# Performance work log

Measured on AMD Instinct MI355X. Metric: run time of the kernel, lower is better.

Reference implementation:

```python
import jax, jax.numpy as jnp
import numpy as np

BN_EPS = 1e-5

def setup_inputs() -> dict:
    key = jax.random.key(0)
    ks = jax.random.split(key, 10)
    B, Cin, Cout, H, W = 4, 256, 128, 64, 64
    Cqk = Cout // 8  # 16
    return {
        "x": jax.random.normal(ks[0], (B, Cin, H, W), dtype=jnp.float32),
        "conv_w": jax.random.normal(ks[1], (Cout, Cin, 3, 3), dtype=jnp.float32) * 0.03,
        "bn_gamma": jnp.ones((Cout,), dtype=jnp.float32),
        "bn_beta": jnp.zeros((Cout,), dtype=jnp.float32),
        "q_w": jax.random.normal(ks[2], (Cqk, Cout), dtype=jnp.float32) * 0.05,
        "q_b": jnp.zeros((Cqk,), dtype=jnp.float32),
        "k_w": jax.random.normal(ks[3], (Cqk, Cout), dtype=jnp.float32) * 0.05,
        "k_b": jnp.zeros((Cqk,), dtype=jnp.float32),
        "v_w": jax.random.normal(ks[4], (Cout, Cout), dtype=jnp.float32) * 0.05,
        "v_b": jnp.zeros((Cout,), dtype=jnp.float32),
        # gamma params are zero-init in the original; use small nonzero values so the
        # attention branches actually contribute (better correctness signal).
        "gamma_ca": jax.random.normal(ks[5], (1,), dtype=jnp.float32) * 0.1,
        "gamma_pa": jax.random.normal(ks[6], (1,), dtype=jnp.float32) * 0.1,
    }

def _conv_bn_relu(x, conv_w, bn_gamma, bn_beta):
    # 3x3 conv, stride 1, pad 1, no bias (NCHW / OIHW)
    y = jax.lax.conv_general_dilated(
        x, conv_w, window_strides=(1, 1), padding=((1, 1), (1, 1)),
        dimension_numbers=("NCHW", "OIHW", "NCHW"))
    # BatchNorm2d in training mode: batch statistics over (N, H, W)
    mean = jnp.mean(y, axis=(0, 2, 3), keepdims=True)
    var = jnp.var(y, axis=(0, 2, 3), keepdims=True)
    y = (y - mean) * jax.lax.rsqrt(var + BN_EPS)
    y = y * bn_gamma[None, :, None, None] + bn_beta[None, :, None, None]
    return jax.nn.relu(y)

def _cam(feat, gamma):
    B, C, H, W = feat.shape
    f = feat.reshape(B, C, H * W)                       # (B, C, N)
    energy = jnp.einsum("bcn,bdn->bcd", f, f)           # (B, C, C)
    energy_new = jnp.max(energy, axis=-1, keepdims=True) - energy
    attn = jnp.tanh(energy_new)
    out = jnp.einsum("bcd,bdn->bcn", attn, f).reshape(B, C, H, W)
    return gamma * out + feat

def _pam(feat, q_w, q_b, k_w, k_b, v_w, v_b, gamma):
    B, C, H, W = feat.shape
    N = H * W
    f = feat.reshape(B, C, N)
    q = jnp.einsum("oc,bcn->bon", q_w, f) + q_b[None, :, None]   # (B, C//8, N)
    k = jnp.einsum("oc,bcn->bon", k_w, f) + k_b[None, :, None]
    v = jnp.einsum("oc,bcn->bon", v_w, f) + v_b[None, :, None]   # (B, C, N)
    energy = jnp.einsum("bqn,bqm->bnm", q, k)                    # (B, N, N)
    attn = jnp.tanh(energy)
    # torch: bmm(value, attention^T): out[b,c,m] = sum_n v[b,c,n] * attn[b,m,n]
    out = jnp.einsum("bcn,bmn->bcm", v, attn).reshape(B, C, H, W)
    return gamma * out + feat

def reference(x, conv_w, bn_gamma, bn_beta, q_w, q_b, k_w, k_b, v_w, v_b, gamma_ca, gamma_pa):
    feat = _conv_bn_relu(x, conv_w, bn_gamma, bn_beta)
    out_ca = _cam(feat, gamma_ca)
    out_sa = _pam(feat, q_w, q_b, k_w, k_b, v_w, v_b, gamma_pa)
    return out_ca + out_sa + feat
```

## Files before the change

kernel.cpp:

```cpp
#include <hip/hip_runtime.h>
#include <math.h>

#define BATCH 4
#define CIN   256
#define CCH   128
#define HW    4096
#define CQK   16

using short8   = __attribute__((ext_vector_type(8))) short;
using floatx4  = __attribute__((ext_vector_type(4))) float;
using floatx16 = __attribute__((ext_vector_type(16))) float;
using uint4v   = __attribute__((ext_vector_type(4))) unsigned int;

__device__ __forceinline__ float fast_tanh(float x) {
    float e = __builtin_amdgcn_exp2f(x * 2.8853900817779268f);
    float r = __builtin_amdgcn_rcpf(e + 1.0f);
    return __builtin_fmaf(-2.0f, r, 1.0f);
}

__device__ __forceinline__ unsigned short f2bf(float f) {
    unsigned u = __float_as_uint(f);
    u += 0x7fff + ((u >> 16) & 1);
    return (unsigned short)(u >> 16);
}

__device__ __forceinline__ float bf2f(unsigned short u) {
    return __uint_as_float(((unsigned)u) << 16);
}

#define ROWMAP(r, hi) (((r) & 3) + (((r) >> 2) << 3) + ((hi) << 2))

#define XTP_ROW   (66 * 256)
#define XTP_BATCH (66 * 66 * 256)

__global__ __launch_bounds__(256) void prep_all_kernel(
        const float* __restrict__ x, const float* __restrict__ w,
        const float* __restrict__ qw, const float* __restrict__ qb,
        const float* __restrict__ kw, const float* __restrict__ kb,
        const float* __restrict__ vw, const float* __restrict__ vb,
        unsigned short* __restrict__ xTp, unsigned short* __restrict__ Wb2,
        unsigned short* __restrict__ Wqkv, float* __restrict__ biasAll,
        float* __restrict__ statsS, float* __restrict__ statsQ) {
    const int bx = blockIdx.x, tid = threadIdx.x;
    if (bx < 1024) {
        __shared__ unsigned short lds[64][72];
        const int ci0 = (bx & 3) << 6, yr = (bx >> 2) & 63, b = bx >> 8;
        const int cir = tid >> 2, xc = tid & 3;
        const float* xp = x + (((b << 8) + ci0 + cir) << 12) + (yr << 6) + xc * 16;
#pragma unroll
        for (int j = 0; j < 4; ++j) {
            float4 v = *(const float4*)(xp + j * 4);
            int xi = xc * 16 + j * 4;
            lds[xi + 0][cir] = f2bf(v.x);
            lds[xi + 1][cir] = f2bf(v.y);
            lds[xi + 2][cir] = f2bf(v.z);
            lds[xi + 3][cir] = f2bf(v.w);
        }
        const short8 z8 = (short8){0,0,0,0,0,0,0,0};
        if (tid < 16) {
            int col = (tid >> 3) ? 65 : 0;
            int part = tid & 7;
            *(short8*)(xTp + b * XTP_BATCH + (yr + 1) * XTP_ROW + col * 256 +
                       ci0 + part * 8) = z8;
        }
        if (yr == 0 || yr == 63) {
            int row = (yr == 0) ? 0 : 65;
            for (int e = tid; e < 528; e += 256) {
                int xi = e >> 3, part = e & 7;
                *(short8*)(xTp + b * XTP_BATCH + row * XTP_ROW + xi * 256 +
                           ci0 + part * 8) = z8;
            }
        }
        __syncthreads();
        const int xr = tid >> 2, part = tid & 3;
        unsigned short* dst = xTp + b * XTP_BATCH + (yr + 1) * XTP_ROW +
                              (xr + 1) * 256 + ci0 + part * 16;
        *(short8*)(dst + 0) = *(const short8*)&lds[xr][part * 16 + 0];
        *(short8*)(dst + 8) = *(const short8*)&lds[xr][part * 16 + 8];
    } else if (bx < 2176) {
        int o = (bx - 1024) * 256 + tid;
        int s   = o & 31;
        int co  = (o >> 5) & 127;
        int cc  = (o >> 12) & 7;
        int tap = o >> 15;
        int ci  = (cc << 5) + s;
        Wb2[o] = f2bf(w[co * 2304 + ci * 9 + tap]);
    } else if (bx < 2256) {
        int idx = (bx - 2176) * 256 + tid;
        int o = idx >> 7, c = idx & 127;
        float wv = (o < 16) ? qw[(o << 7) + c]
                 : (o < 32) ? kw[((o - 16) << 7) + c]
                            : vw[((o - 32) << 7) + c];
        Wqkv[idx] = f2bf(wv);
        if (idx < 160)
            biasAll[idx] = (idx < 16) ? qb[idx] : (idx < 32) ? kb[idx - 16] : vb[idx - 32];
    } else {
        if (tid < 128) { statsS[tid] = 0.f; statsQ[tid] = 0.f; }
    }
}

#define LOADBAND(R, KY)                                                        \
    {                                                                          \
        const unsigned short* g_ = bandbase + (KY) * XTP_ROW;                  \
        _Pragma("unroll")                                                      \
        for (int j = 0; j < 4; ++j)                                            \
            R[j] = *(const short8*)(g_ + ((tid + j * 256) << 3));              \
        if (tid < 64) R[4] = *(const short8*)(g_ + ((1024 + tid) << 3));       \
    }

#define WRITEBAND(R, BUF)                                                      \
    {                                                                          \
        char* p_ = (char*)&Bl[BUF][0];                                         \
        _Pragma("unroll")                                                      \
        for (int j = 0; j < 4; ++j) {                                          \
            int bb_ = (tid + j * 256) << 4;                                    \
            *(short8*)(p_ + (bb_ ^ (((bb_ >> 9) & 7) << 4))) = R[j];           \
        }                                                                      \
        if (tid < 64) {                                                        \
            int bb_ = (1024 + tid) << 4;                                       \
            *(short8*)(p_ + (bb_ ^ (((bb_ >> 9) & 7) << 4))) = R[4];           \
        }                                                                      \
    }

#define LOADA(P, TAP)                                                          \
    {                                                                          \
        const unsigned short* ar_ = Wb2 + ((TAP) << 15) + (aco0 << 5) + (quad << 3); \
        _Pragma("unroll")                                                      \
        for (int cc = 0; cc < 8; ++cc) {                                       \
            P[2 * cc]     = *(const short8*)(ar_ + (cc << 12));                \
            P[2 * cc + 1] = *(const short8*)(ar_ + (cc << 12) + 512);          \
        }                                                                      \
    }

#define CONVSTEP(BUF, KX, PC, PN, TAPN, PREF)                                  \
    {                                                                          \
        const char* bp_ = (const char*)&Bl[BUF][0];                            \
        const int pl0_ = l15 + (KX);                                           \
        const int sw_ = (pl0_ & 7) << 4;                                       \
        const int b0_ = (pl0_ << 9) + (quad << 4);                             \
        const int b1_ = b0_ + (16 << 9);                                       \
        const unsigned short* arn_ = Wb2 + ((TAPN) << 15) + (aco0 << 5) + (quad << 3); \
        _Pragma("unroll")                                                      \
        for (int cc = 0; cc < 8; ++cc) {                                       \
            if (PREF) {                                                        \
                PN[2 * cc]     = *(const short8*)(arn_ + (cc << 12));          \
                PN[2 * cc + 1] = *(const short8*)(arn_ + (cc << 12) + 512);    \
            }                                                                  \
            short8 bf0 = *(const short8*)(bp_ + ((b0_ + (cc << 6)) ^ sw_));    \
            short8 bf1 = *(const short8*)(bp_ + ((b1_ + (cc << 6)) ^ sw_));    \
            acc00 = __builtin_amdgcn_mfma_f32_16x16x32_bf16(PC[2 * cc], bf0, acc00, 0, 0, 0); \
            acc01 = __builtin_amdgcn_mfma_f32_16x16x32_bf16(PC[2 * cc], bf1, acc01, 0, 0, 0); \
            acc10 = __builtin_amdgcn_mfma_f32_16x16x32_bf16(PC[2 * cc + 1], bf0, acc10, 0, 0, 0); \
            acc11 = __builtin_amdgcn_mfma_f32_16x16x32_bf16(PC[2 * cc + 1], bf1, acc11, 0, 0, 0); \
        }                                                                      \
    }

__global__ __launch_bounds__(256, 2) void conv_mfma_kernel(
        const unsigned short* __restrict__ xTp, const unsigned short* __restrict__ Wb2,
        float* __restrict__ y, float* __restrict__ convP) {
    const int tid = threadIdx.x;
    const int w = tid >> 6, lane = tid & 63, l15 = lane & 15, quad = lane >> 4;
    const int idx = blockIdx.x;
    const int xcd = idx & 7, rr = idx >> 3;
    const int yl = rr & 7, ph = (rr >> 3) & 1, b = rr >> 4;
    const int yr = (xcd << 3) + yl;
    const int cobase = w << 5;
    const int px0 = ph << 5;
    const int aco0 = cobase + l15;

    __shared__ __align__(16) unsigned short Bl[2][8704];

    const unsigned short* bandbase = xTp + b * XTP_BATCH + yr * XTP_ROW + (px0 << 8);

    floatx4 acc00 = (floatx4){0.f, 0.f, 0.f, 0.f};
    floatx4 acc01 = (floatx4){0.f, 0.f, 0.f, 0.f};
    floatx4 acc10 = (floatx4){0.f, 0.f, 0.f, 0.f};
    floatx4 acc11 = (floatx4){0.f, 0.f, 0.f, 0.f};

    short8 r0[5], r1[5], r2[5];
    short8 AbA[16], AbB[16];

    LOADBAND(r0, 0);
    WRITEBAND(r0, 0);
    LOADBAND(r1, 1);
    LOADA(AbA, 0);
    __syncthreads();

    WRITEBAND(r1, 1);
    LOADBAND(r2, 2);
    CONVSTEP(0, 0, AbA, AbB, 1, 1)
    CONVSTEP(0, 1, AbB, AbA, 2, 1)
    CONVSTEP(0, 2, AbA, AbB, 3, 1)
    __syncthreads();

    WRITEBAND(r2, 0);
    CONVSTEP(1, 0, AbB, AbA, 4, 1)
    CONVSTEP(1, 1, AbA, AbB, 5, 1)
    CONVSTEP(1, 2, AbB, AbA, 6, 1)
    __syncthreads();

    CONVSTEP(0, 0, AbA, AbB, 7, 1)
    CONVSTEP(0, 1, AbB, AbA, 8, 1)
    CONVSTEP(0, 2, AbA, AbB, 0, 0)

#pragma unroll
    for (int ns = 0; ns < 2; ++ns) {
        int px = px0 + (ns << 4) + l15;
        floatx4 a0 = ns ? acc01 : acc00;
        floatx4 a1 = ns ? acc11 : acc10;
#pragma unroll
        for (int r = 0; r < 4; ++r) {
            int co0 = cobase + (quad << 2) + r;
            y[(((b << 7) + co0) << 12) + (yr << 6) + px] = a0[r];
            y[(((b << 7) + co0 + 16) << 12) + (yr << 6) + px] = a1[r];
        }
    }

#pragma unroll
    for (int ms = 0; ms < 2; ++ms) {
        floatx4 aa = ms ? acc10 : acc00;
        floatx4 ab = ms ? acc11 : acc01;
#pragma unroll
        for (int r = 0; r < 4; ++r) {
            float s = aa[r] + ab[r];
            float q = aa[r] * aa[r] + ab[r] * ab[r];
#pragma unroll
            for (int off = 1; off < 16; off <<= 1) {
                s += __shfl_xor(s, off);
                q += __shfl_xor(q, off);
            }
            if (l15 == 0) {
                int co = cobase + ms * 16 + (quad << 2) + r;
                convP[(co << 9) + idx] = s;
                convP[((128 + co) << 9) + idx] = q;
            }
        }
    }
}

__global__ __launch_bounds__(64) void stats_reduce_kernel(
        const float* __restrict__ convP, float* __restrict__ statsS,
        float* __restrict__ statsQ) {
    const int s = blockIdx.x, t = threadIdx.x;
    const float* p = convP + (s << 9);
    float v = 0.f;
#pragma unroll
    for (int j = 0; j < 8; ++j) v += p[t + (j << 6)];
#pragma unroll
    for (int off = 32; off; off >>= 1) v += __shfl_xor(v, off);
    if (t == 0) {
        if (s < 128) statsS[s] = v;
        else         statsQ[s - 128] = v;
    }
}

__global__ __launch_bounds__(256) void bn_apply_kernel(
        const float* __restrict__ y, const float* __restrict__ statsS,
        const float* __restrict__ statsQ, const float* __restrict__ gamma,
        const float* __restrict__ beta, unsigned short* __restrict__ featB,
        unsigned short* __restrict__ fT) {
    __shared__ unsigned short lds[64][72];
    const int tid = threadIdx.x;
    const int c0 = blockIdx.x * 64, n0 = blockIdx.y * 64, b = blockIdx.z;
    const int cir = tid >> 2, xc = tid & 3;
    const int c = c0 + cir;
    const float S = statsS[c], Q = statsQ[c];
    const float mean = S * (1.f / 16384.f);
    const float var  = Q * (1.f / 16384.f) - mean * mean;
    const float rstd = rsqrtf(var + 1e-5f);
    const float sc = gamma[c] * rstd;
    const float sh = beta[c] - mean * sc;
    const float* yp = y + (((b << 7) + c) << 12) + n0 + xc * 16;
    unsigned short* fp = featB + (((b << 7) + c) << 12) + n0 + xc * 16;
#pragma unroll
    for (int j = 0; j < 4; ++j) {
        float4 v = *(const float4*)(yp + j * 4);
        ushort4 o;
        o.x = f2bf(fmaxf(fmaf(v.x, sc, sh), 0.f));
        o.y = f2bf(fmaxf(fmaf(v.y, sc, sh), 0.f));
        o.z = f2bf(fmaxf(fmaf(v.z, sc, sh), 0.f));
        o.w = f2bf(fmaxf(fmaf(v.w, sc, sh), 0.f));
        *(ushort4*)(fp + j * 4) = o;
        int ni = xc * 16 + j * 4;
        lds[ni + 0][cir] = o.x;
        lds[ni + 1][cir] = o.y;
        lds[ni + 2][cir] = o.z;
        lds[ni + 3][cir] = o.w;
    }
    __syncthreads();
    const int nr = tid >> 2, part = tid & 3;
    unsigned short* dst = fT + (((b << 12) + n0 + nr) << 7) + c0 + part * 16;
    *(short8*)(dst + 0) = *(const short8*)&lds[nr][part * 16 + 0];
    *(short8*)(dst + 8) = *(const short8*)&lds[nr][part * 16 + 8];
}

__global__ __launch_bounds__(256) void camqkv_kernel(
        const unsigned short* __restrict__ featB, float* __restrict__ ep,
        const unsigned short* __restrict__ Wqkv, const float* __restrict__ biasAll,
        const unsigned short* __restrict__ fT,
        unsigned short* __restrict__ qT, unsigned short* __restrict__ kT,
        unsigned short* __restrict__ vB) {
    const int bx = blockIdx.x, tid = threadIdx.x;
    const int l31 = tid & 31, hi = (tid >> 5) & 1;
    if (bx < 256) {
        const int kc = bx & 63, b = bx >> 6, wv = tid >> 6;
        floatx16 acc[4];
#pragma unroll
        for (int t = 0; t < 4; ++t)
#pragma unroll
            for (int r = 0; r < 16; ++r) acc[t][r] = 0.f;
        for (int s = 0; s < 4; ++s) {
            const int k0 = (kc << 6) + (s << 4) + (hi << 3);
            short8 fr = *(const short8*)&featB[(((b << 7) + (wv << 5) + l31) << 12) + k0];
            short8 fc0 = *(const short8*)&featB[(((b << 7) +  0 + l31) << 12) + k0];
            short8 fc1 = *(const short8*)&featB[(((b << 7) + 32 + l31) << 12) + k0];
            short8 fc2 = *(const short8*)&featB[(((b << 7) + 64 + l31) << 12) + k0];
            short8 fc3 = *(const short8*)&featB[(((b << 7) + 96 + l31) << 12) + k0];
            acc[0] = __builtin_amdgcn_mfma_f32_32x32x16_bf16(fr, fc0, acc[0], 0, 0, 0);
            acc[1] = __builtin_amdgcn_mfma_f32_32x32x16_bf16(fr, fc1, acc[1], 0, 0, 0);
            acc[2] = __builtin_amdgcn_mfma_f32_32x32x16_bf16(fr, fc2, acc[2], 0, 0, 0);
            acc[3] = __builtin_amdgcn_mfma_f32_32x32x16_bf16(fr, fc3, acc[3], 0, 0, 0);
        }
#pragma unroll
        for (int t = 0; t < 4; ++t)
#pragma unroll
            for (int r = 0; r < 16; ++r) {
                int c = ((tid >> 6) << 5) + ROWMAP(r, hi);
                int d = (t << 5) + l31;
                ep[(((kc << 2) + b) << 14) + (c << 7) + d] = acc[t][r];
            }
    } else {
        const int bi = bx - 256, b = bi >> 6, w = tid >> 6;
        const int n0 = ((bi & 63) << 6) + ((w >> 1) << 5);
        const int tstart = (w & 1) ? 3 : 0;
        const int tcnt   = (w & 1) ? 2 : 3;
        floatx16 acc[3];
#pragma unroll
        for (int t = 0; t < 3; ++t)
#pragma unroll
            for (int r = 0; r < 16; ++r) acc[t][r] = 0.f;
        for (int s = 0; s < 8; ++s) {
            const int k0 = (s << 4) + (hi << 3);
            short8 bf = *(const short8*)&fT[(((b << 12) + n0 + l31) << 7) + k0];
#pragma unroll
            for (int ti = 0; ti < 3; ++ti) {
                if (ti < tcnt) {
                    short8 aw = *(const short8*)&Wqkv[((((tstart + ti) << 5) + l31) << 7) + k0];
                    acc[ti] = __builtin_amdgcn_mfma_f32_32x32x16_bf16(aw, bf, acc[ti], 0, 0, 0);
                }
            }
        }
        const int n = n0 + l31;
#pragma unroll
        for (int ti = 0; ti < 3; ++ti) {
            if (ti >= tcnt) continue;
            const int t = tstart + ti;
#pragma unroll
            for (int r = 0; r < 16; ++r) {
                int o = (t << 5) + ROWMAP(r, hi);
                float val = acc[ti][r] + biasAll[o];
                if (t == 0) {
                    if (o < 16) qT[(((b << 12) + n) << 4) + o] = f2bf(val);
                    else        kT[(((b << 12) + n) << 4) + o - 16] = f2bf(val);
                } else if (o >= 32) {
                    vB[(((b << 7) + o - 32) << 12) + n] = f2bf(val);
                }
            }
        }
    }
}

#define PAM_STEP(LB, NC)                                                          \
    {                                                                             \
        const unsigned short* lb_ = (LB);                                         \
        const int na_ = nbase + ((NC) << 5);                                      \
        short8 avl0 = *(const short8*)(lb_ + ( l31       * 40) + hi * 8);         \
        short8 avh0 = *(const short8*)(lb_ + ( l31       * 40) + 16 + hi * 8);    \
        short8 avl1 = *(const short8*)(lb_ + ((32 + l31) * 40) + hi * 8);         \
        short8 avh1 = *(const short8*)(lb_ + ((32 + l31) * 40) + 16 + hi * 8);    \
        short8 avl2 = *(const short8*)(lb_ + ((64 + l31) * 40) + hi * 8);         \
        short8 avh2 = *(const short8*)(lb_ + ((64 + l31) * 40) + 16 + hi * 8);    \
        short8 avl3 = *(const short8*)(lb_ + ((96 + l31) * 40) + hi * 8);         \
        short8 avh3 = *(const short8*)(lb_ + ((96 + l31) * 40) + 16 + hi * 8);    \
        floatx16 s_ = __builtin_amdgcn_mfma_f32_32x32x16_bf16(ak, bq, zero16, 0, 0, 0); \
        if ((NC) < 31)                                                            \
            ak = *(const short8*)&kT[(((b << 12) + na_ + 32 + l31) << 4) + hi * 8]; \
        unsigned p_[8];                                                           \
        _Pragma("unroll")                                                         \
        for (int i = 0; i < 8; ++i) {                                             \
            float t0 = fast_tanh(s_[2 * i]);                                      \
            float t1 = fast_tanh(s_[2 * i + 1]);                                  \
            p_[i] = (__float_as_uint(t1) & 0xFFFF0000u) | (__float_as_uint(t0) >> 16); \
        }                                                                         \
        unsigned q0 = p_[0], q1 = p_[1], q2 = p_[2], q3 = p_[3];                  \
        unsigned q4 = p_[4], q5 = p_[5], q6 = p_[6], q7 = p_[7];                  \
        asm("v_permlane32_swap_b32 %0, %1" : "+v"(q0), "+v"(q2));                 \
        asm("v_permlane32_swap_b32 %0, %1" : "+v"(q1), "+v"(q3));                 \
        asm("v_permlane32_swap_b32 %0, %1" : "+v"(q4), "+v"(q6));                 \
        asm("v_permlane32_swap_b32 %0, %1" : "+v"(q5), "+v"(q7));                 \
        uint4v b1u, b2u;                                                          \
        b1u[0] = q0; b1u[1] = q1; b1u[2] = q2; b1u[3] = q3;                       \
        b2u[0] = q4; b2u[1] = q5; b2u[2] = q6; b2u[3] = q7;                       \
        short8 B1 = __builtin_bit_cast(short8, b1u);                              \
        short8 B2 = __builtin_bit_cast(short8, b2u);                              \
        __builtin_amdgcn_s_setprio(1);                                            \
        acc[0] = __builtin_amdgcn_mfma_f32_32x32x16_bf16(avl0, B1, acc[0], 0, 0, 0); \
        acc[0] = __builtin_amdgcn_mfma_f32_32x32x16_bf16(avh0, B2, acc[0], 0, 0, 0); \
        acc[1] = __builtin_amdgcn_mfma_f32_32x32x16_bf16(avl1, B1, acc[1], 0, 0, 0); \
        acc[1] = __builtin_amdgcn_mfma_f32_32x32x16_bf16(avh1, B2, acc[1], 0, 0, 0); \
        acc[2] = __builtin_amdgcn_mfma_f32_32x32x16_bf16(avl2, B1, acc[2], 0, 0, 0); \
        acc[2] = __builtin_amdgcn_mfma_f32_32x32x16_bf16(avh2, B2, acc[2], 0, 0, 0); \
        acc[3] = __builtin_amdgcn_mfma_f32_32x32x16_bf16(avl3, B1, acc[3], 0, 0, 0); \
        acc[3] = __builtin_amdgcn_mfma_f32_32x32x16_bf16(avh3, B2, acc[3], 0, 0, 0); \
        __builtin_amdgcn_s_setprio(0);                                            \
    }

__global__ __launch_bounds__(256) void pam_attn_kernel(
        const unsigned short* __restrict__ qT, const unsigned short* __restrict__ kT,
        const unsigned short* __restrict__ vB, unsigned short* __restrict__ pamP,
        const float* __restrict__ ep, unsigned short* __restrict__ attnB) {
    const int bx = blockIdx.x, tid = threadIdx.x;
    if (bx < 512) {
        const int nh = bx & 3, b = bx >> 7;
        const int w = tid >> 6, lane = tid & 63, l31 = lane & 31, hi = lane >> 5;
        const int m0 = (((bx >> 2) & 31) << 7) + (w << 5);

        __shared__ __align__(16) unsigned short vtile[2][5120];

        short8 bq = *(const short8*)&qT[(((b << 12) + m0 + l31) << 4) + hi * 8];

        floatx16 acc[4], zero16;
#pragma unroll
        for (int r = 0; r < 16; ++r) {
            acc[0][r] = 0.f; acc[1][r] = 0.f; acc[2][r] = 0.f; acc[3][r] = 0.f;
            zero16[r] = 0.f;
        }

        const int nbase = nh << 10;

        const int srow = tid >> 1, shalf = tid & 1;
        const unsigned short* vg = vB + (((b << 7) + srow) << 12) + nbase + shalf * 16;
        unsigned short* sw0 = &vtile[0][srow * 40 + shalf * 16];
        unsigned short* sw1 = &vtile[1][srow * 40 + shalf * 16];

        short8 ak = *(const short8*)&kT[(((b << 12) + nbase + l31) << 4) + hi * 8];

        short8 gA0 = *(const short8*)(vg + 0);
        short8 gA1 = *(const short8*)(vg + 8);
        short8 gB0 = *(const short8*)(vg + 32);
        short8 gB1 = *(const short8*)(vg + 40);
        *(short8*)(sw0 + 0) = gA0;
        *(short8*)(sw0 + 8) = gA1;

        for (int t = 0; t < 16; ++t) {
            const int e = t << 1;
            __syncthreads();
            *(short8*)(sw1 + 0) = gB0;
            *(short8*)(sw1 + 8) = gB1;
            if (t < 15) {
                gA0 = *(const short8*)(vg + (e + 2) * 32);
                gA1 = *(const short8*)(vg + (e + 2) * 32 + 8);
            }
            PAM_STEP(&vtile[0][0], e);
            __syncthreads();
            if (t < 15) {
                *(short8*)(sw0 + 0) = gA0;
                *(short8*)(sw0 + 8) = gA1;
                gB0 = *(const short8*)(vg + (e + 3) * 32);
                gB1 = *(const short8*)(vg + (e + 3) * 32 + 8);
            }
            PAM_STEP(&vtile[1][0], e + 1);
        }

        const int pbase = (((nh << 2) + b) << 19) + m0 + l31;
#pragma unroll
        for (int ct = 0; ct < 4; ++ct)
#pragma unroll
            for (int r = 0; r < 16; ++r) {
                int c = (ct << 5) + ROWMAP(r, hi);
                pamP[pbase + (c << 12)] = f2bf(acc[ct][r]);
            }
    } else {
        const int bi = bx - 512, b = bi >> 6;
        const int half = tid >> 7, t = tid & 127;
        const int c = ((bi & 63) << 1) + half;
        float v = 0.f;
#pragma unroll 8
        for (int s = 0; s < 64; ++s)
            v += ep[(((s << 2) + b) << 14) + (c << 7) + t];
        float m = v;
        for (int off = 32; off; off >>= 1) m = fmaxf(m, __shfl_down(m, off));
        __shared__ float mx[4];
        if ((tid & 63) == 0) mx[tid >> 6] = m;
        __syncthreads();
        float M = fmaxf(mx[half << 1], mx[(half << 1) + 1]);
        attnB[(b << 14) + (c << 7) + t] = f2bf(fast_tanh(M - v));
    }
}

__global__ __launch_bounds__(256) void combine_kernel(
        const unsigned short* __restrict__ attnB, const unsigned short* __restrict__ fT,
        const unsigned short* __restrict__ featB, const unsigned short* __restrict__ pamP,
        const float* __restrict__ gca, const float* __restrict__ gpa,
        float* __restrict__ out) {
    const int b = blockIdx.y, tid = threadIdx.x;
    const int w = tid >> 6, l31 = tid & 31, hi = (tid >> 5) & 1;
    const int m0 = (blockIdx.x << 6) + ((w >> 1) << 5);
    const int ct0 = (w & 1) << 1;
    floatx16 acc[2];
#pragma unroll
    for (int t = 0; t < 2; ++t)
#pragma unroll
        for (int r = 0; r < 16; ++r) acc[t][r] = 0.f;

    for (int s = 0; s < 8; ++s) {
        const int k0 = (s << 4) + (hi << 3);
        short8 bf = *(const short8*)&fT[(((b << 12) + m0 + l31) << 7) + k0];
        short8 a0 = *(const short8*)&attnB[(b << 14) + ((((ct0 + 0) << 5) + l31) << 7) + k0];
        short8 a1 = *(const short8*)&attnB[(b << 14) + ((((ct0 + 1) << 5) + l31) << 7) + k0];
        acc[0] = __builtin_amdgcn_mfma_f32_32x32x16_bf16(a0, bf, acc[0], 0, 0, 0);
        acc[1] = __builtin_amdgcn_mfma_f32_32x32x16_bf16(a1, bf, acc[1], 0, 0, 0);
    }
    const float gc = gca[0], gp = gpa[0];
    const int m = m0 + l31;
#pragma unroll
    for (int t = 0; t < 2; ++t)
#pragma unroll
        for (int r = 0; r < 16; ++r) {
            int c = ((ct0 + t) << 5) + ROWMAP(r, hi);
            int ci = (c << 12) + m;
            float p = bf2f(pamP[((0 * 4 + b) << 19) + ci]) +
                      bf2f(pamP[((1 * 4 + b) << 19) + ci]) +
                      bf2f(pamP[((2 * 4 + b) << 19) + ci]) +
                      bf2f(pamP[((3 * 4 + b) << 19) + ci]);
            float fb = bf2f(featB[(((b << 7) + c) << 12) + m]);
            out[(((b << 7) + c) << 12) + m] = 3.f * fb + gc * acc[t][r] + gp * p;
        }
}

extern "C" void kernel_launch(void* const* d_in, const int* in_sizes, int n_in,
                              void* d_out, int out_size, void* d_ws, size_t ws_size,
                              hipStream_t stream) {
    const float* x      = (const float*)d_in[0];
    const float* conv_w = (const float*)d_in[1];
    const float* bn_g   = (const float*)d_in[2];
    const float* bn_b   = (const float*)d_in[3];
    const float* q_w    = (const float*)d_in[4];
    const float* q_b    = (const float*)d_in[5];
    const float* k_w    = (const float*)d_in[6];
    const float* k_b    = (const float*)d_in[7];
    const float* v_w    = (const float*)d_in[8];
    const float* v_b    = (const float*)d_in[9];
    const float* gca    = (const float*)d_in[10];
    const float* gpa    = (const float*)d_in[11];
    float* out = (float*)d_out;

    float* ws = (float*)d_ws;
    float* convY  = ws;
    unsigned short* xTp = (unsigned short*)(ws + 2097152);
    float* ep     = ws + 4327424;
    unsigned short* Wb2  = (unsigned short*)(ws + 8521728);
    unsigned short* Wqkv = (unsigned short*)(ws + 8669184);
    float* statsS  = ws + 8679424;
    float* statsQ  = ws + 8679552;
    float* biasAll = ws + 8679680;
    unsigned short* attnB = (unsigned short*)(ws + 8679872);
    unsigned short* qT    = (unsigned short*)(ws + 8712640);
    unsigned short* kT    = (unsigned short*)(ws + 8843712);
    unsigned short* vB    = (unsigned short*)(ws + 8974784);
    unsigned short* featB = (unsigned short*)(ws + 10023360);
    unsigned short* fT    = (unsigned short*)(ws + 11071936);
    float* convP = ws + 4327424;
    unsigned short* pamP  = (unsigned short*)ws;

    prep_all_kernel<<<2257, 256, 0, stream>>>(x, conv_w, q_w, q_b, k_w, k_b,
                                              v_w, v_b, xTp, Wb2, Wqkv, biasAll,
                                              statsS, statsQ);
    conv_mfma_kernel<<<512, 256, 0, stream>>>(xTp, Wb2, convY, convP);
    stats_reduce_kernel<<<256, 64, 0, stream>>>(convP, statsS, statsQ);
    bn_apply_kernel<<<dim3(2, 64, 4), 256, 0, stream>>>(convY, statsS, statsQ,
                                                        bn_g, bn_b, featB, fT);
    camqkv_kernel<<<512, 256, 0, stream>>>(featB, ep, Wqkv, biasAll, fT, qT, kT, vB);
    pam_attn_kernel<<<768, 256, 0, stream>>>(qT, kT, vB, pamP, ep, attnB);
    combine_kernel<<<dim3(64, 4), 256, 0, stream>>>(attnB, fT, featB, pamP, gca, gpa, out);
}
```

Before: 171.8 us.

## Process two key chunks per pipeline stage to halve barriers and overlap tanh with MFMA

The PAM attention loop now stages two 32-column V chunks per shared-memory buffer and processes them in one step, halving the number of __syncthreads barriers. Inside a step, the second QK MFMA is issued before the first chunk's PV MFMAs, and its tanh runs afterwards, so VALU tanh work can overlap with matrix-core work. Shared memory per block doubles and register pressure rises from holding two sets of V fragments and scores, which may reduce occupancy.

```diff
diff --git a/kernel.cpp b/kernel.cpp
--- a/kernel.cpp
+++ b/kernel.cpp
@@ -370,48 +370,86 @@
     }
 }
 
-#define PAM_STEP(LB, NC)                                                          \
+#define PAM_STEP2(LB, NC0)                                                        \
     {                                                                             \
-        const unsigned short* lb_ = (LB);                                         \
-        const int na_ = nbase + ((NC) << 5);                                      \
-        short8 avl0 = *(const short8*)(lb_ + ( l31       * 40) + hi * 8);         \
-        short8 avh0 = *(const short8*)(lb_ + ( l31       * 40) + 16 + hi * 8);    \
-        short8 avl1 = *(const short8*)(lb_ + ((32 + l31) * 40) + hi * 8);         \
-        short8 avh1 = *(const short8*)(lb_ + ((32 + l31) * 40) + 16 + hi * 8);    \
-        short8 avl2 = *(const short8*)(lb_ + ((64 + l31) * 40) + hi * 8);         \
-        short8 avh2 = *(const short8*)(lb_ + ((64 + l31) * 40) + 16 + hi * 8);    \
-        short8 avl3 = *(const short8*)(lb_ + ((96 + l31) * 40) + hi * 8);         \
-        short8 avh3 = *(const short8*)(lb_ + ((96 + l31) * 40) + 16 + hi * 8);    \
-        floatx16 s_ = __builtin_amdgcn_mfma_f32_32x32x16_bf16(ak, bq, zero16, 0, 0, 0); \
-        if ((NC) < 31)                                                            \
-            ak = *(const short8*)&kT[(((b << 12) + na_ + 32 + l31) << 4) + hi * 8]; \
-        unsigned p_[8];                                                           \
+        const unsigned short* lbA_ = (LB);                                        \
+        const unsigned short* lbB_ = (LB) + 5120;                                 \
+        short8 aAl0 = *(const short8*)(lbA_ + ( l31       * 40) + hi * 8);        \
+        short8 aAh0 = *(const short8*)(lbA_ + ( l31       * 40) + 16 + hi * 8);   \
+        short8 aAl1 = *(const short8*)(lbA_ + ((32 + l31) * 40) + hi * 8);        \
+        short8 aAh1 = *(const short8*)(lbA_ + ((32 + l31) * 40) + 16 + hi * 8);   \
+        short8 aAl2 = *(const short8*)(lbA_ + ((64 + l31) * 40) + hi * 8);        \
+        short8 aAh2 = *(const short8*)(lbA_ + ((64 + l31) * 40) + 16 + hi * 8);   \
+        short8 aAl3 = *(const short8*)(lbA_ + ((96 + l31) * 40) + hi * 8);        \
+        short8 aAh3 = *(const short8*)(lbA_ + ((96 + l31) * 40) + 16 + hi * 8);   \
+        floatx16 sA_ = __builtin_amdgcn_mfma_f32_32x32x16_bf16(ak, bq, zero16, 0, 0, 0); \
+        ak = *(const short8*)&kT[(((b << 12) + nbase + (((NC0) + 1) << 5) + l31) << 4) + hi * 8]; \
+        short8 aBl0 = *(const short8*)(lbB_ + ( l31       * 40) + hi * 8);        \
+        short8 aBh0 = *(const short8*)(lbB_ + ( l31       * 40) + 16 + hi * 8);   \
+        short8 aBl1 = *(const short8*)(lbB_ + ((32 + l31) * 40) + hi * 8);        \
+        short8 aBh1 = *(const short8*)(lbB_ + ((32 + l31) * 40) + 16 + hi * 8);   \
+        short8 aBl2 = *(const short8*)(lbB_ + ((64 + l31) * 40) + hi * 8);        \
+        short8 aBh2 = *(const short8*)(lbB_ + ((64 + l31) * 40) + 16 + hi * 8);   \
+        short8 aBl3 = *(const short8*)(lbB_ + ((96 + l31) * 40) + hi * 8);        \
+        short8 aBh3 = *(const short8*)(lbB_ + ((96 + l31) * 40) + 16 + hi * 8);   \
+        unsigned pA_[8];                                                          \
         _Pragma("unroll")                                                         \
         for (int i = 0; i < 8; ++i) {                                             \
-            float t0 = fast_tanh(s_[2 * i]);                                      \
-            float t1 = fast_tanh(s_[2 * i + 1]);                                  \
-            p_[i] = (__float_as_uint(t1) & 0xFFFF0000u) | (__float_as_uint(t0) >> 16); \
+            float t0 = fast_tanh(sA_[2 * i]);                                     \
+            float t1 = fast_tanh(sA_[2 * i + 1]);                                 \
+            pA_[i] = (__float_as_uint(t1) & 0xFFFF0000u) | (__float_as_uint(t0) >> 16); \
         }                                                                         \
-        unsigned q0 = p_[0], q1 = p_[1], q2 = p_[2], q3 = p_[3];                  \
-        unsigned q4 = p_[4], q5 = p_[5], q6 = p_[6], q7 = p_[7];                  \
-        asm("v_permlane32_swap_b32 %0, %1" : "+v"(q0), "+v"(q2));                 \
-        asm("v_permlane32_swap_b32 %0, %1" : "+v"(q1), "+v"(q3));                 \
-        asm("v_permlane32_swap_b32 %0, %1" : "+v"(q4), "+v"(q6));                 \
-        asm("v_permlane32_swap_b32 %0, %1" : "+v"(q5), "+v"(q7));                 \
-        uint4v b1u, b2u;                                                          \
-        b1u[0] = q0; b1u[1] = q1; b1u[2] = q2; b1u[3] = q3;                       \
-        b2u[0] = q4; b2u[1] = q5; b2u[2] = q6; b2u[3] = q7;                       \
-        short8 B1 = __builtin_bit_cast(short8, b1u);                              \
-        short8 B2 = __builtin_bit_cast(short8, b2u);                              \
+        unsigned a0 = pA_[0], a1 = pA_[1], a2 = pA_[2], a3 = pA_[3];              \
+        unsigned a4 = pA_[4], a5 = pA_[5], a6 = pA_[6], a7 = pA_[7];              \
+        asm("v_permlane32_swap_b32 %0, %1" : "+v"(a0), "+v"(a2));                 \
+        asm("v_permlane32_swap_b32 %0, %1" : "+v"(a1), "+v"(a3));                 \
+        asm("v_permlane32_swap_b32 %0, %1" : "+v"(a4), "+v"(a6));                 \
+        asm("v_permlane32_swap_b32 %0, %1" : "+v"(a5), "+v"(a7));                 \
+        uint4v b1uA, b2uA;                                                        \
+        b1uA[0] = a0; b1uA[1] = a1; b1uA[2] = a2; b1uA[3] = a3;                   \
+        b2uA[0] = a4; b2uA[1] = a5; b2uA[2] = a6; b2uA[3] = a7;                   \
+        short8 B1A = __builtin_bit_cast(short8, b1uA);                            \
+        short8 B2A = __builtin_bit_cast(short8, b2uA);                            \
+        floatx16 sB_ = __builtin_amdgcn_mfma_f32_32x32x16_bf16(ak, bq, zero16, 0, 0, 0); \
+        if ((NC0) + 2 < 32)                                                       \
+            ak = *(const short8*)&kT[(((b << 12) + nbase + (((NC0) + 2) << 5) + l31) << 4) + hi * 8]; \
         __builtin_amdgcn_s_setprio(1);                                            \
-        acc[0] = __builtin_amdgcn_mfma_f32_32x32x16_bf16(avl0, B1, acc[0], 0, 0, 0); \
-        acc[0] = __builtin_amdgcn_mfma_f32_32x32x16_bf16(avh0, B2, acc[0], 0, 0, 0); \
-        acc[1] = __builtin_amdgcn_mfma_f32_32x32x16_bf16(avl1, B1, acc[1], 0, 0, 0); \
-        acc[1] = __builtin_amdgcn_mfma_f32_32x32x16_bf16(avh1, B2, acc[1], 0, 0, 0); \
-        acc[2] = __builtin_amdgcn_mfma_f32_32x32x16_bf16(avl2, B1, acc[2], 0, 0, 0); \
-        acc[2] = __builtin_amdgcn_mfma_f32_32x32x16_bf16(avh2, B2, acc[2], 0, 0, 0); \
-        acc[3] = __builtin_amdgcn_mfma_f32_32x32x16_bf16(avl3, B1, acc[3], 0, 0, 0); \
-        acc[3] = __builtin_amdgcn_mfma_f32_32x32x16_bf16(avh3, B2, acc[3], 0, 0, 0); \
+        acc[0] = __builtin_amdgcn_mfma_f32_32x32x16_bf16(aAl0, B1A, acc[0], 0, 0, 0); \
+        acc[0] = __builtin_amdgcn_mfma_f32_32x32x16_bf16(aAh0, B2A, acc[0], 0, 0, 0); \
+        acc[1] = __builtin_amdgcn_mfma_f32_32x32x16_bf16(aAl1, B1A, acc[1], 0, 0, 0); \
+        acc[1] = __builtin_amdgcn_mfma_f32_32x32x16_bf16(aAh1, B2A, acc[1], 0, 0, 0); \
+        acc[2] = __builtin_amdgcn_mfma_f32_32x32x16_bf16(aAl2, B1A, acc[2], 0, 0, 0); \
+        acc[2] = __builtin_amdgcn_mfma_f32_32x32x16_bf16(aAh2, B2A, acc[2], 0, 0, 0); \
+        acc[3] = __builtin_amdgcn_mfma_f32_32x32x16_bf16(aAl3, B1A, acc[3], 0, 0, 0); \
+        acc[3] = __builtin_amdgcn_mfma_f32_32x32x16_bf16(aAh3, B2A, acc[3], 0, 0, 0); \
+        __builtin_amdgcn_s_setprio(0);                                            \
+        unsigned pB_[8];                                                          \
+        _Pragma("unroll")                                                         \
+        for (int i = 0; i < 8; ++i) {                                             \
+            float t0 = fast_tanh(sB_[2 * i]);                                     \
+            float t1 = fast_tanh(sB_[2 * i + 1]);                                 \
+            pB_[i] = (__float_as_uint(t1) & 0xFFFF0000u) | (__float_as_uint(t0) >> 16); \
+        }                                                                         \
+        unsigned c0_ = pB_[0], c1_ = pB_[1], c2_ = pB_[2], c3_ = pB_[3];          \
+        unsigned c4_ = pB_[4], c5_ = pB_[5], c6_ = pB_[6], c7_ = pB_[7];          \
+        asm("v_permlane32_swap_b32 %0, %1" : "+v"(c0_), "+v"(c2_));               \
+        asm("v_permlane32_swap_b32 %0, %1" : "+v"(c1_), "+v"(c3_));               \
+        asm("v_permlane32_swap_b32 %0, %1" : "+v"(c4_), "+v"(c6_));               \
+        asm("v_permlane32_swap_b32 %0, %1" : "+v"(c5_), "+v"(c7_));               \
+        uint4v b1uB, b2uB;                                                        \
+        b1uB[0] = c0_; b1uB[1] = c1_; b1uB[2] = c2_; b1uB[3] = c3_;               \
+        b2uB[0] = c4_; b2uB[1] = c5_; b2uB[2] = c6_; b2uB[3] = c7_;               \
+        short8 B1B = __builtin_bit_cast(short8, b1uB);                            \
+        short8 B2B = __builtin_bit_cast(short8, b2uB);                            \
+        __builtin_amdgcn_s_setprio(1);                                            \
+        acc[0] = __builtin_amdgcn_mfma_f32_32x32x16_bf16(aBl0, B1B, acc[0], 0, 0, 0); \
+        acc[0] = __builtin_amdgcn_mfma_f32_32x32x16_bf16(aBh0, B2B, acc[0], 0, 0, 0); \
+        acc[1] = __builtin_amdgcn_mfma_f32_32x32x16_bf16(aBl1, B1B, acc[1], 0, 0, 0); \
+        acc[1] = __builtin_amdgcn_mfma_f32_32x32x16_bf16(aBh1, B2B, acc[1], 0, 0, 0); \
+        acc[2] = __builtin_amdgcn_mfma_f32_32x32x16_bf16(aBl2, B1B, acc[2], 0, 0, 0); \
+        acc[2] = __builtin_amdgcn_mfma_f32_32x32x16_bf16(aBh2, B2B, acc[2], 0, 0, 0); \
+        acc[3] = __builtin_amdgcn_mfma_f32_32x32x16_bf16(aBl3, B1B, acc[3], 0, 0, 0); \
+        acc[3] = __builtin_amdgcn_mfma_f32_32x32x16_bf16(aBh3, B2B, acc[3], 0, 0, 0); \
         __builtin_amdgcn_s_setprio(0);                                            \
     }
 
@@ -425,7 +463,7 @@
         const int w = tid >> 6, lane = tid & 63, l31 = lane & 31, hi = lane >> 5;
         const int m0 = (((bx >> 2) & 31) << 7) + (w << 5);
 
-        __shared__ __align__(16) unsigned short vtile[2][5120];
+        __shared__ __align__(16) unsigned short vtile[2][10240];
 
         short8 bq = *(const short8*)&qT[(((b << 12) + m0 + l31) << 4) + hi * 8];
 
@@ -440,36 +478,52 @@
 
         const int srow = tid >> 1, shalf = tid & 1;
         const unsigned short* vg = vB + (((b << 7) + srow) << 12) + nbase + shalf * 16;
-        unsigned short* sw0 = &vtile[0][srow * 40 + shalf * 16];
-        unsigned short* sw1 = &vtile[1][srow * 40 + shalf * 16];
+        unsigned short* sw0t0 = &vtile[0][srow * 40 + shalf * 16];
+        unsigned short* sw0t1 = &vtile[0][5120 + srow * 40 + shalf * 16];
+        unsigned short* sw1t0 = &vtile[1][srow * 40 + shalf * 16];
+        unsigned short* sw1t1 = &vtile[1][5120 + srow * 40 + shalf * 16];
 
         short8 ak = *(const short8*)&kT[(((b << 12) + nbase + l31) << 4) + hi * 8];
 
         short8 gA0 = *(const short8*)(vg + 0);
         short8 gA1 = *(const short8*)(vg + 8);
-        short8 gB0 = *(const short8*)(vg + 32);
-        short8 gB1 = *(const short8*)(vg + 40);
-        *(short8*)(sw0 + 0) = gA0;
-        *(short8*)(sw0 + 8) = gA1;
-
-        for (int t = 0; t < 16; ++t) {
-            const int e = t << 1;
+        short8 gA2 = *(const short8*)(vg + 32);
+        short8 gA3 = *(const short8*)(vg + 40);
+        short8 gB0 = *(const short8*)(vg + 64);
+        short8 gB1 = *(const short8*)(vg + 72);
+        short8 gB2 = *(const short8*)(vg + 96);
+        short8 gB3 = *(const short8*)(vg + 104);
+        *(short8*)(sw0t0 + 0) = gA0;
+        *(short8*)(sw0t0 + 8) = gA1;
+        *(short8*)(sw0t1 + 0) = gA2;
+        *(short8*)(sw0t1 + 8) = gA3;
+
+        for (int t = 0; t < 8; ++t) {
+            const int e0 = t << 2;
             __syncthreads();
-            *(short8*)(sw1 + 0) = gB0;
-            *(short8*)(sw1 + 8) = gB1;
-            if (t < 15) {
-                gA0 = *(const short8*)(vg + (e + 2) * 32);
-                gA1 = *(const short8*)(vg + (e + 2) * 32 + 8);
-            }
-            PAM_STEP(&vtile[0][0], e);
+            *(short8*)(sw1t0 + 0) = gB0;
+            *(short8*)(sw1t0 + 8) = gB1;
+            *(short8*)(sw1t1 + 0) = gB2;
+            *(short8*)(sw1t1 + 8) = gB3;
+            if (t < 7) {
+                gA0 = *(const short8*)(vg + (e0 + 4) * 32);
+                gA1 = *(const short8*)(vg + (e0 + 4) * 32 + 8);
+                gA2 = *(const short8*)(vg + (e0 + 5) * 32);
+                gA3 = *(const short8*)(vg + (e0 + 5) * 32 + 8);
+            }
+            PAM_STEP2(&vtile[0][0], e0);
             __syncthreads();
-            if (t < 15) {
-                *(short8*)(sw0 + 0) = gA0;
-                *(short8*)(sw0 + 8) = gA1;
-                gB0 = *(const short8*)(vg + (e + 3) * 32);
-                gB1 = *(const short8*)(vg + (e + 3) * 32 + 8);
-            }
-            PAM_STEP(&vtile[1][0], e + 1);
+            if (t < 7) {
+                *(short8*)(sw0t0 + 0) = gA0;
+                *(short8*)(sw0t0 + 8) = gA1;
+                *(short8*)(sw0t1 + 0) = gA2;
+                *(short8*)(sw0t1 + 8) = gA3;
+                gB0 = *(const short8*)(vg + (e0 + 6) * 32);
+                gB1 = *(const short8*)(vg + (e0 + 6) * 32 + 8);
+                gB2 = *(const short8*)(vg + (e0 + 7) * 32);
+                gB3 = *(const short8*)(vg + (e0 + 7) * 32 + 8);
+            }
+            PAM_STEP2(&vtile[1][0], e0 + 2);
         }
 
         const int pbase = (((nh << 2) + b) << 19) + m0 + l31;
```

Result: no change. 175.0 us (+1.9%).
